# Optimization experiments

Hardware: AMD Instinct MI355X
Metric: run time of the kernel (lower is better)

## Reference

```python
import jax, jax.numpy as jnp
import numpy as np

DIM = 2048
KV_DIM = 1024
NUM_HEADS = 16
HEAD_DIM = DIM // NUM_HEADS  # 128
EPS = 1e-6
B, LQ, LKV = 2, 4096, 1024


def _rope_cos_sin(L, d, base=10000.0):
    inv_freq = 1.0 / (base ** (np.arange(0, d, 2, dtype=np.float32) / d))  # [d/2]
    freqs = np.arange(L, dtype=np.float32)[:, None] * inv_freq[None, :]   # [L, d/2]
    emb = np.concatenate([freqs, freqs], axis=-1)                          # [L, d]
    return jnp.asarray(np.cos(emb)), jnp.asarray(np.sin(emb))


def setup_inputs() -> dict:
    key = jax.random.key(0)
    ks = jax.random.split(key, 10)
    x = jax.random.normal(ks[0], (B, LQ, DIM), dtype=jnp.float32)
    y = jax.random.normal(ks[1], (B, LKV, KV_DIM), dtype=jnp.float32)
    xc, xs = _rope_cos_sin(LQ, HEAD_DIM)
    yc, ys = _rope_cos_sin(LKV, HEAD_DIM)
    x_cos = jnp.broadcast_to(xc[None], (B, LQ, HEAD_DIM))
    x_sin = jnp.broadcast_to(xs[None], (B, LQ, HEAD_DIM))
    y_cos = jnp.broadcast_to(yc[None], (B, LKV, HEAD_DIM))
    y_sin = jnp.broadcast_to(ys[None], (B, LKV, HEAD_DIM))
    s = 0.02
    Wq = jax.random.normal(ks[2], (DIM, DIM), dtype=jnp.float32) * s
    Wk = jax.random.normal(ks[3], (DIM, KV_DIM), dtype=jnp.float32) * s
    Wv = jax.random.normal(ks[4], (DIM, KV_DIM), dtype=jnp.float32) * s
    Wo = jax.random.normal(ks[5], (DIM, DIM), dtype=jnp.float32) * s
    bq = jnp.zeros((DIM,), jnp.float32)
    bk = jnp.zeros((DIM,), jnp.float32)
    bv = jnp.zeros((DIM,), jnp.float32)
    bo = jnp.zeros((DIM,), jnp.float32)
    rmsq_w = jnp.ones((DIM,), jnp.float32)
    rmsk_w = jnp.ones((DIM,), jnp.float32)
    ln_w = jnp.ones((KV_DIM,), jnp.float32)
    ln_b = jnp.zeros((KV_DIM,), jnp.float32)
    return dict(x=x, y=y, x_cos=x_cos, x_sin=x_sin, y_cos=y_cos, y_sin=y_sin,
                Wq=Wq, bq=bq, Wk=Wk, bk=bk, Wv=Wv, bv=bv, Wo=Wo, bo=bo,
                rmsq_w=rmsq_w, rmsk_w=rmsk_w, ln_w=ln_w, ln_b=ln_b)


def _rms_norm(t, w, eps=EPS):
    return t * jax.lax.rsqrt(jnp.mean(t * t, axis=-1, keepdims=True) + eps) * w


def _layer_norm(t, w, b, eps=EPS):
    mu = jnp.mean(t, axis=-1, keepdims=True)
    var = jnp.mean(jnp.square(t - mu), axis=-1, keepdims=True)
    return (t - mu) * jax.lax.rsqrt(var + eps) * w + b


def _rotate_half(t):
    d2 = t.shape[-1] // 2
    return jnp.concatenate([-t[..., d2:], t[..., :d2]], axis=-1)


def _apply_rope(t, cos, sin):
    # t: [B, L, H, D]; cos/sin: [B, L, D] -> unsqueeze head dim (unsqueeze_dim=2)
    cos = cos[:, :, None, :]
    sin = sin[:, :, None, :]
    return t * cos + _rotate_half(t) * sin


def _block_forward(x, y, x_cos, x_sin, y_cos, y_sin,
                   Wq, bq, Wk, bk, Wv, bv, Wo, bo,
                   rmsq_w, rmsk_w, ln_w, ln_b):
    Bb, Lq, D = x.shape
    Lk = y.shape[1]
    H, Dh = NUM_HEADS, HEAD_DIM
    # y pre-norm (block-level LayerNorm)
    yn = _layer_norm(y, ln_w, ln_b)
    # projections + RMSNorm on q/k
    q = _rms_norm(x @ Wq.T + bq, rmsq_w)   # [B, Lq, D]
    k = _rms_norm(yn @ Wk.T + bk, rmsk_w)  # [B, Lk, D]
    v = yn @ Wv.T + bv                     # [B, Lk, D]
    # split heads and apply RoPE
    q = _apply_rope(q.reshape(Bb, Lq, H, Dh), x_cos, x_sin)
    k = _apply_rope(k.reshape(Bb, Lk, H, Dh), y_cos, y_sin)
    v = v.reshape(Bb, Lk, H, Dh)
    # non-causal cross attention, scale = 1/sqrt(head_dim)
    scale = 1.0 / jnp.sqrt(jnp.asarray(Dh, q.dtype))
    scores = jnp.einsum('blhd,bmhd->bhlm', q, k) * scale
    probs = jax.nn.softmax(scores, axis=-1)
    out = jnp.einsum('bhlm,bmhd->blhd', probs, v).reshape(Bb, Lq, D)
    return out @ Wo.T + bo


def reference(x, y, x_cos, x_sin, y_cos, y_sin,
              Wq, bq, Wk, bk, Wv, bv, Wo, bo,
              rmsq_w, rmsk_w, ln_w, ln_b):
    return _block_forward(x, y, x_cos, x_sin, y_cos, y_sin,
                          Wq, bq, Wk, bk, Wv, bv, Wo, bo,
                          rmsq_w, rmsk_w, ln_w, ln_b)
```

## Files before the change

### kernel.cpp

```cpp
#include <hip/hip_runtime.h>


typedef __attribute__((ext_vector_type(8))) short    short8;
typedef __attribute__((ext_vector_type(8))) unsigned short ushort8;
typedef __attribute__((ext_vector_type(4))) unsigned short ushort4v;
typedef __attribute__((ext_vector_type(4))) float    f32x4;
typedef __attribute__((ext_vector_type(16))) float   f32x16;
typedef __attribute__((ext_vector_type(4))) unsigned int uint4v;

#define DEV __device__ __forceinline__

DEV unsigned short f2bf(float f) {
  unsigned int u = __builtin_bit_cast(unsigned int, f);
  u += 0x7FFFu + ((u >> 16) & 1u);
  return (unsigned short)(u >> 16);
}
DEV float bf2f(unsigned short h) {
  return __builtin_bit_cast(float, ((unsigned int)h) << 16);
}
DEV unsigned int cvtpk_bf16(float lo, float hi) {
  unsigned int r;
  asm("v_cvt_pk_bf16_f32 %0, %1, %2" : "=v"(r) : "v"(lo), "v"(hi));
  return r;
}
DEV short8 mk8(unsigned a, unsigned b, unsigned c, unsigned d) {
  uint4v t; t.x = a; t.y = b; t.z = c; t.w = d;
  return __builtin_bit_cast(short8, t);
}

DEV void gload_lds16(const void* g, void* l) {
  __builtin_amdgcn_global_load_lds(
      (const __attribute__((address_space(1))) void*)g,
      (__attribute__((address_space(3))) void*)l, 16, 0, 0);
}

__global__ __launch_bounds__(256) void prep_kernel(const float* __restrict__ y,
                                                   const float* __restrict__ lnw,
                                                   const float* __restrict__ lnb,
                                                   unsigned short* __restrict__ yn,
                                                   const float* __restrict__ x,
                                                   const float* __restrict__ Wq,
                                                   const float* __restrict__ Wk,
                                                   const float* __restrict__ Wv,
                                                   const float* __restrict__ Wo,
                                                   unsigned short* __restrict__ xb,
                                                   unsigned short* __restrict__ Wqb,
                                                   unsigned short* __restrict__ Wkb,
                                                   unsigned short* __restrict__ Wvb,
                                                   unsigned short* __restrict__ Wob) {
  const int t = threadIdx.x;
  if (blockIdx.x < 2048) {
    const int row = blockIdx.x;
    const float* yr = y + (size_t)row * 1024;
    float4 v = *(const float4*)(yr + t * 4);
    float s1 = v.x + v.y + v.z + v.w;
    float s2 = v.x * v.x + v.y * v.y + v.z * v.z + v.w * v.w;
#pragma unroll
    for (int m = 1; m < 64; m <<= 1) {
      s1 += __shfl_xor(s1, m);
      s2 += __shfl_xor(s2, m);
    }
    __shared__ float red[8];
    const int wave = t >> 6, lane = t & 63;
    if (lane == 0) { red[wave] = s1; red[4 + wave] = s2; }
    __syncthreads();
    s1 = red[0] + red[1] + red[2] + red[3];
    s2 = red[4] + red[5] + red[6] + red[7];
    const float mu = s1 * (1.0f / 1024.0f);
    const float var = s2 * (1.0f / 1024.0f) - mu * mu;
    const float rs = rsqrtf(var + 1e-6f);
    ushort4v o;
    o.x = f2bf((v.x - mu) * rs * lnw[t * 4 + 0] + lnb[t * 4 + 0]);
    o.y = f2bf((v.y - mu) * rs * lnw[t * 4 + 1] + lnb[t * 4 + 1]);
    o.z = f2bf((v.z - mu) * rs * lnw[t * 4 + 2] + lnb[t * 4 + 2]);
    o.w = f2bf((v.w - mu) * rs * lnw[t * 4 + 3] + lnb[t * 4 + 3]);
    *(ushort4v*)(yn + (size_t)row * 1024 + t * 4) = o;
    return;
  }
  const int nx = 4194304, nwq = 1048576, nwk = 524288, nwv = 524288;
  const int total = 7340032;
  int i = (blockIdx.x - 2048) * 256 + t;
  const int stride = 1536 * 256;
  for (; i < total; i += stride) {
    int j = i;
    const float* s; unsigned short* d;
    if (j < nx) { s = x; d = xb; }
    else if ((j -= nx) < nwq) { s = Wq; d = Wqb; }
    else if ((j -= nwq) < nwk) { s = Wk; d = Wkb; }
    else if ((j -= nwk) < nwv) { s = Wv; d = Wvb; }
    else { j -= nwv; s = Wo; d = Wob; }
    float4 v = *(const float4*)(s + (size_t)j * 4);
    ushort4v o;
    o.x = f2bf(v.x); o.y = f2bf(v.y); o.z = f2bf(v.z); o.w = f2bf(v.w);
    *(ushort4v*)(d + (size_t)j * 4) = o;
  }
}

template <int EPI>
DEV void gemm256_body(const unsigned short* __restrict__ A,
                      const unsigned short* __restrict__ W,
                      const float* __restrict__ bias0,
                      const float* __restrict__ bias1,
                      int nsplit, void* __restrict__ Cout,
                      int M, int N, int K, int ldRow,
                      int bidLocal, int nwg, char* ldsb, int tid) {
  const int wave = tid >> 6, lane = tid & 63;
  const int l31 = lane & 31, hi = lane >> 5;
  const int wm = wave >> 2, wn = wave & 3;

  const int wgid = (bidLocal & 7) * (nwg >> 3) + (bidLocal >> 3);
  const int nbn = N >> 8;
  const int m0 = (wgid / nbn) * 256;
  const int n0 = (wgid % nbn) * 256;

  const char* Ab = (const char*)A;
  const char* Wb = (const char*)W;
  const size_t ld = (size_t)ldRow * 2;
  const int NT = K >> 6;
  const int NI = NT >> 1;

  const int prow2 = tid >> 4;
  const int psw   = ((tid * 16) & 255) ^ ((prow2 & 15) << 4);
  const int pdst  = tid * 16;
  const char* pAg = Ab + (size_t)(m0 + 2 * prow2 + (psw >> 7)) * ld + (psw & 127);
  const char* pBg = Wb + (size_t)(n0 + 2 * prow2 + (psw >> 7)) * ld + (psw & 127);

  f32x16 acc[4][2] = {};
  short8 af[2][4];
  short8 bf[2][4];

#define LDSB(BUF, SEG) (ldsb + ((BUF) * 4 + (SEG)) * 16384)

#define STG(BUF, HALF, ISB, TAU) do {                                         \
    const char* _g = ((ISB) ? pBg : pAg) + (size_t)(HALF) * 128 * ld +        \
                     (size_t)(TAU) * 128;                                     \
    char* _l = LDSB(BUF, (ISB) * 2 + (HALF));                                 \
    gload_lds16(_g, _l + pdst);                                               \
    gload_lds16(_g + 64 * ld, _l + pdst + 8192);                              \
  } while (0)

#define LDA(BUF, H) do {                                                      \
    const char* _b = LDSB(BUF, wm);                                           \
    _Pragma("unroll") for (int mf = 0; mf < 2; ++mf) {                        \
      const int ar = (H) * 64 + mf * 32 + l31;                                \
      const int _r = ar >> 1;                                                 \
      const int swz = (_r & 15) << 4;                                         \
      _Pragma("unroll") for (int ks = 0; ks < 4; ++ks)                        \
        af[mf][ks] = *(const short8*)(_b + _r * 256 +                         \
                       (((ar & 1) * 128 + ks * 32 + hi * 16) ^ swz));         \
    }                                                                         \
  } while (0)

#define LDB(BUF, G) do {                                                      \
    const char* _b = LDSB(BUF, 2 + (wn >> 1));                                \
    const int br = (wn & 1) * 64 + (G) * 32 + l31;                            \
    const int _r = br >> 1;                                                   \
    const int swz = (_r & 15) << 4;                                           \
    _Pragma("unroll") for (int ks = 0; ks < 4; ++ks)                          \
      bf[G][ks] = *(const short8*)(_b + _r * 256 +                            \
                     (((br & 1) * 128 + ks * 32 + hi * 16) ^ swz));           \
  } while (0)

#define MFMA_Q(H, G) do {                                                     \
    __builtin_amdgcn_s_setprio(1);                                            \
    _Pragma("unroll") for (int ks = 0; ks < 4; ++ks)                          \
    _Pragma("unroll") for (int mf = 0; mf < 2; ++mf)                          \
      acc[(H) * 2 + mf][G] =                                                  \
        __builtin_amdgcn_mfma_f32_32x32x16_bf16(af[mf][ks], bf[G][ks],        \
                                                acc[(H) * 2 + mf][G], 0,0,0); \
    __builtin_amdgcn_s_setprio(0);                                            \
  } while (0)

#define BAR() __builtin_amdgcn_s_barrier()
#define VM4() asm volatile("s_waitcnt vmcnt(4)" ::: "memory")
#define VM0() asm volatile("s_waitcnt vmcnt(0)" ::: "memory")

  STG(0, 0, 0, 0); STG(0, 1, 0, 0); STG(0, 0, 1, 0); STG(0, 1, 1, 0);
  STG(1, 0, 1, 1); STG(1, 1, 1, 1);
  VM4(); BAR();

  for (int t = 0; t < NI - 1; ++t) {
    const int t2 = 2 * t;
    LDA(0, 0); LDB(0, 0); STG(1, 0, 0, t2 + 1);
    BAR(); MFMA_Q(0, 0); BAR();
    LDB(0, 1); STG(1, 1, 0, t2 + 1);
    BAR(); MFMA_Q(0, 1); BAR();
    LDA(0, 1); STG(0, 0, 1, t2 + 2);
    BAR(); MFMA_Q(1, 1); BAR();
    STG(0, 1, 1, t2 + 2);
    BAR(); MFMA_Q(1, 0); VM4(); BAR();
    LDA(1, 0); LDB(1, 0); STG(0, 0, 0, t2 + 2);
    BAR(); MFMA_Q(0, 0); BAR();
    LDB(1, 1); STG(0, 1, 0, t2 + 2);
    BAR(); MFMA_Q(0, 1); BAR();
    LDA(1, 1); STG(1, 0, 1, t2 + 3);
    BAR(); MFMA_Q(1, 1); BAR();
    STG(1, 1, 1, t2 + 3);
    BAR(); MFMA_Q(1, 0); VM4(); BAR();
  }

  LDA(0, 0); LDB(0, 0); STG(1, 0, 0, NT - 1);
  BAR(); MFMA_Q(0, 0); BAR();
  LDB(0, 1); STG(1, 1, 0, NT - 1);
  BAR(); MFMA_Q(0, 1); BAR();
  LDA(0, 1);
  BAR(); MFMA_Q(1, 1); BAR();
  BAR(); MFMA_Q(1, 0); VM0(); BAR();
  LDA(1, 0); LDB(1, 0); MFMA_Q(0, 0);
  LDB(1, 1); MFMA_Q(0, 1);
  LDA(1, 1); MFMA_Q(1, 1);
  MFMA_Q(1, 0);

#undef STG
#undef LDA
#undef LDB
#undef MFMA_Q
#undef BAR
#undef VM4
#undef VM0
#undef LDSB

#pragma unroll
  for (int nf = 0; nf < 2; ++nf) {
    const int n = n0 + wn * 64 + nf * 32 + l31;
    float bv = 0.f;
    if constexpr (EPI != 2) bv = (n < nsplit) ? bias0[n] : bias1[n - nsplit];
#pragma unroll
    for (int mfr = 0; mfr < 4; ++mfr) {
      const int mB = m0 + wm * 128 + mfr * 32 + 4 * hi;
#pragma unroll
      for (int r = 0; r < 16; ++r) {
        const int row = mB + (r & 3) + 8 * (r >> 2);
        const float v = acc[mfr][nf][r] + bv;
        if constexpr (EPI == 1)
          ((float*)Cout)[(size_t)row * N + n] = v;
        else
          ((unsigned short*)Cout)[(size_t)row * N + n] = f2bf(v);
      }
    }
  }
}

__global__ __launch_bounds__(512, 2) void gemm_dual(const unsigned short* __restrict__ xb,
                                                    const unsigned short* __restrict__ Wqb,
                                                    const float* __restrict__ bq,
                                                    unsigned short* __restrict__ qpre,
                                                    const unsigned short* __restrict__ ynb,
                                                    const unsigned short* __restrict__ Wkb,
                                                    unsigned short* __restrict__ kvpA,
                                                    unsigned short* __restrict__ kvpB) {
  __shared__ __align__(16) char lds[2][4][16384];
  gemm256_body<0>(xb, Wqb, bq, bq, 2048, qpre, 8192, 2048, 2048, 2048,
                  blockIdx.x, 256, &lds[0][0][0], threadIdx.x);
  __syncthreads();
  const int kvt = blockIdx.x & 127, khalf = blockIdx.x >> 7;
  gemm256_body<2>(ynb + khalf * 512, Wkb + khalf * 512, nullptr, nullptr, 0,
                  khalf ? kvpB : kvpA, 2048, 4096, 512, 1024,
                  kvt, 128, &lds[0][0][0], threadIdx.x);
}

__global__ __launch_bounds__(512, 2) void gemm_f32(const unsigned short* __restrict__ A,
                                                   const unsigned short* __restrict__ W,
                                                   const float* __restrict__ bias,
                                                   float* __restrict__ C,
                                                   int M, int N, int K) {
  __shared__ __align__(16) char lds[2][4][16384];
  gemm256_body<1>(A, W, bias, bias, N, C, M, N, K, K,
                  blockIdx.x, 256, &lds[0][0][0], threadIdx.x);
}

DEV void rmsrope2_body(const unsigned short* __restrict__ in,
                       const unsigned short* __restrict__ in2,
                       const float* __restrict__ bias,
                       const float* __restrict__ w,
                       const float* __restrict__ cs,
                       const float* __restrict__ sn,
                       unsigned short* __restrict__ out,
                       int L, int ldin, float scale, int row,
                       float* srow, float* red) {
  const int t = threadIdx.x;
  ushort8 v = *(const ushort8*)(in + (size_t)row * ldin + t * 8);
  float vals[8];
  if (in2) {
    ushort8 v2 = *(const ushort8*)(in2 + (size_t)row * ldin + t * 8);
#pragma unroll
    for (int j = 0; j < 8; ++j) vals[j] = bf2f(v[j]) + bf2f(v2[j]) + bias[t * 8 + j];
  } else {
#pragma unroll
    for (int j = 0; j < 8; ++j) vals[j] = bf2f(v[j]);
  }
  float ss = 0.f;
#pragma unroll
  for (int j = 0; j < 8; ++j) { ss += vals[j] * vals[j]; srow[t * 8 + j] = vals[j]; }
#pragma unroll
  for (int m = 1; m < 64; m <<= 1) ss += __shfl_xor(ss, m);
  const int wave = t >> 6, lane = t & 63;
  if (lane == 0) red[wave] = ss;
  __syncthreads();
  const float tot = red[0] + red[1] + red[2] + red[3];
  const float rms = rsqrtf(tot * (1.0f / 2048.0f) + 1e-6f);

  const int n0 = t * 8;
  const int d0 = n0 & 127;
  const int hh = n0 >> 7;
  const float sign = (d0 < 64) ? -1.0f : 1.0f;
  const float* cb = cs + (size_t)row * 128 + d0;
  const float* sb = sn + (size_t)row * 128 + d0;
  ushort8 ou;
#pragma unroll
  for (int j = 0; j < 8; ++j) {
    const float self = vals[j] * rms * w[n0 + j];
    const float part = srow[(n0 ^ 64) + j] * rms * w[(n0 ^ 64) + j];
    ou[j] = f2bf((self * cb[j] + sign * part * sb[j]) * scale);
  }
  const int b = row / L, l = row - (row / L) * L;
  *(ushort8*)(out + (((size_t)(b * 16 + hh)) * L + l) * 128 + d0) = ou;
}

DEV void vtrans2_body(const unsigned short* __restrict__ va,
                      const unsigned short* __restrict__ vb,
                      const float* __restrict__ bv,
                      unsigned short* __restrict__ vt, int ldv, int bid,
                      unsigned short (*lt)[130]) {
  const int kt = bid & 15, bh = bid >> 4;
  const int h = bh & 15, b = bh >> 4;
  const int t = threadIdx.x;
  const int i0 = t >> 4, c0 = (t & 15) * 8;
  const size_t sbase = ((size_t)(b * 1024 + kt * 64)) * ldv + h * 128;
#pragma unroll
  for (int ii = 0; ii < 4; ++ii) {
    const int i = i0 + ii * 16;
    ushort8 a = *(const ushort8*)(va + sbase + (size_t)i * ldv + c0);
    ushort8 bb = *(const ushort8*)(vb + sbase + (size_t)i * ldv + c0);
#pragma unroll
    for (int j = 0; j < 8; ++j)
      lt[i][c0 + j] = f2bf(bf2f(a[j]) + bf2f(bb[j]) + bv[h * 128 + c0 + j]);
  }
  __syncthreads();
  const int d0 = t >> 3, j0 = (t & 7) * 8;
  unsigned short* dst = vt + (size_t)bh * 128 * 1024 + kt * 64;
#pragma unroll
  for (int dd = 0; dd < 4; ++dd) {
    const int d = d0 + dd * 32;
    ushort8 o;
#pragma unroll
    for (int jj = 0; jj < 8; ++jj) o[jj] = lt[j0 + jj][d];
    *(ushort8*)(dst + (size_t)d * 1024 + j0) = o;
  }
}

__global__ __launch_bounds__(256) void post_kernel(const unsigned short* __restrict__ qpre,
                                                   const float* __restrict__ rmsq_w,
                                                   const float* __restrict__ x_cos,
                                                   const float* __restrict__ x_sin,
                                                   unsigned short* __restrict__ qr,
                                                   const unsigned short* __restrict__ kvpA,
                                                   const unsigned short* __restrict__ kvpB,
                                                   const float* __restrict__ bk,
                                                   const float* __restrict__ bv,
                                                   const float* __restrict__ rmsk_w,
                                                   const float* __restrict__ y_cos,
                                                   const float* __restrict__ y_sin,
                                                   unsigned short* __restrict__ kr,
                                                   unsigned short* __restrict__ vt,
                                                   float qscale) {
  __shared__ __align__(16) float srow[2048];
  __shared__ float red[4];
  __shared__ unsigned short lt[64][130];
  const int b = blockIdx.x;
  if (b < 8192) {
    rmsrope2_body(qpre, nullptr, nullptr, rmsq_w, x_cos, x_sin, qr,
                  4096, 2048, qscale, b, srow, red);
  } else if (b < 10240) {
    rmsrope2_body(kvpA, kvpB, bk, rmsk_w, y_cos, y_sin, kr,
                  1024, 4096, 1.0f, b - 8192, srow, red);
  } else {
    vtrans2_body(kvpA + 2048, kvpB + 2048, bv, vt, 4096, b - 10240, lt);
  }
}

__global__ __launch_bounds__(256, 2) void attn_kernel(const unsigned short* __restrict__ q,
                                                      const unsigned short* __restrict__ k,
                                                      const unsigned short* __restrict__ vt,
                                                      unsigned short* __restrict__ ao) {
  __shared__ __align__(16) char sK[2][64 * 256];
  __shared__ __align__(16) char sV[2][64 * 256];

  const int bid0 = blockIdx.x;
  const int bid = (bid0 & 7) * 128 + (bid0 >> 3);
  const int qt = bid & 31, bh = bid >> 5;
  const int tid = threadIdx.x;
  const int wave = tid >> 6, lane = tid & 63;
  const int l31 = lane & 31, hi = lane >> 5;

  const unsigned short* qbase = q + (((size_t)bh * 4096) + qt * 128 + wave * 32) * 128;
  const char* kbase = (const char*)(k + (size_t)bh * 1024 * 128);
  const char* vbase = (const char*)(vt + (size_t)bh * 128 * 1024);

  short8 qb[8];
#pragma unroll
  for (int step = 0; step < 8; ++step)
    qb[step] = *(const short8*)(qbase + (size_t)l31 * 128 + step * 16 + hi * 8);

  f32x16 o[4] = {};
  float lsum = 0.f;

#define STAGE_KV(BUF, KV0) do {                                              \
    _Pragma("unroll")                                                        \
    for (int i = 0; i < 4; ++i) {                                            \
      const int p = (i * 256 + tid) * 16;                                    \
      const int row = p >> 8;                                                \
      const int si = (p & 255) ^ ((row & 15) << 4);                          \
      gload_lds16(kbase + (size_t)((KV0) + row) * 256 + si, sK[BUF] + p);    \
    }                                                                        \
    _Pragma("unroll")                                                        \
    for (int i = 0; i < 4; ++i) {                                            \
      const int p = (i * 256 + tid) * 16;                                    \
      const int row = p >> 8;                                                \
      const int si = (p & 255) ^ ((row & 15) << 4);                          \
      const int d = 2 * row + (si >> 7);                                     \
      gload_lds16(vbase + (size_t)d * 2048 + (KV0) * 2 + (si & 127),         \
                  sV[BUF] + p);                                              \
    }                                                                        \
  } while (0)

#define QK(K, S0, S1) do {                                                   \
    const int ksw = (l31 & 15) << 4;                                         \
    _Pragma("unroll") for (int step = 0; step < 8; ++step) {                 \
      const int cb2 = step * 32 + hi * 16;                                   \
      short8 kf0 = *(const short8*)((K) + l31 * 256 + (cb2 ^ ksw));          \
      short8 kf1 = *(const short8*)((K) + (32 + l31) * 256 + (cb2 ^ ksw));   \
      S0 = __builtin_amdgcn_mfma_f32_32x32x16_bf16(kf0, qb[step], S0, 0,0,0);\
      S1 = __builtin_amdgcn_mfma_f32_32x32x16_bf16(kf1, qb[step], S1, 0,0,0);\
    }                                                                        \
  } while (0)

#define SOFTMAX_PV(V, SS, F) do {                                            \
    float p_[16];                                                            \
    _Pragma("unroll") for (int r = 0; r < 16; ++r) p_[r] = exp2f((SS)[r]);   \
    lsum += (((p_[0]+p_[1])+(p_[2]+p_[3])) + ((p_[4]+p_[5])+(p_[6]+p_[7])))  \
          + (((p_[8]+p_[9])+(p_[10]+p_[11])) + ((p_[12]+p_[13])+(p_[14]+p_[15])));\
    unsigned w0 = cvtpk_bf16(p_[0], p_[1]),  w1 = cvtpk_bf16(p_[2], p_[3]),  \
             w2 = cvtpk_bf16(p_[4], p_[5]),  w3 = cvtpk_bf16(p_[6], p_[7]),  \
             w4 = cvtpk_bf16(p_[8], p_[9]),  w5 = cvtpk_bf16(p_[10], p_[11]),\
             w6 = cvtpk_bf16(p_[12], p_[13]),w7 = cvtpk_bf16(p_[14], p_[15]);\
    asm volatile("v_permlane32_swap_b32 %0, %1" : "+v"(w0), "+v"(w2));       \
    asm volatile("v_permlane32_swap_b32 %0, %1" : "+v"(w1), "+v"(w3));       \
    asm volatile("v_permlane32_swap_b32 %0, %1" : "+v"(w4), "+v"(w6));       \
    asm volatile("v_permlane32_swap_b32 %0, %1" : "+v"(w5), "+v"(w7));       \
    const short8 fr0 = mk8(w0, w1, w2, w3);                                  \
    const short8 fr1 = mk8(w4, w5, w6, w7);                                  \
    _Pragma("unroll") for (int kstep = 0; kstep < 2; ++kstep) {              \
      const short8 pa = kstep ? fr1 : fr0;                                   \
      const int colb = (F) * 64 + kstep * 32 + hi * 16;                      \
      _Pragma("unroll") for (int dt = 0; dt < 4; ++dt) {                     \
        const int vrow = dt * 16 + (l31 >> 1);                               \
        const int inner = (l31 & 1) * 128 + colb;                            \
        short8 vf = *(const short8*)((V) + vrow * 256 +                      \
                                     (inner ^ ((vrow & 15) << 4)));          \
        o[dt] = __builtin_amdgcn_mfma_f32_32x32x16_bf16(pa, vf, o[dt], 0,0,0);\
      }                                                                      \
    }                                                                        \
  } while (0)

#define TILE(BUF) do {                                                       \
    f32x16 s0 = {}, s1 = {};                                                 \
    QK(sK[BUF], s0, s1);                                                     \
    SOFTMAX_PV(sV[BUF], s0, 0);                                              \
    SOFTMAX_PV(sV[BUF], s1, 1);                                              \
  } while (0)

  STAGE_KV(0, 0);
  __syncthreads();

#pragma unroll 1
  for (int kt2 = 0; kt2 < 8; ++kt2) {
    STAGE_KV(1, (2 * kt2 + 1) * 64);
    TILE(0);
    __syncthreads();
    if (kt2 < 7) STAGE_KV(0, (2 * kt2 + 2) * 64);
    TILE(1);
    __syncthreads();
  }
#undef STAGE_KV
#undef QK
#undef SOFTMAX_PV
#undef TILE

  lsum += __shfl_xor(lsum, 32);
  const float linv = 1.0f / lsum;
  const int b = bh >> 4, h = bh & 15;
#pragma unroll
  for (int r = 0; r < 16; ++r) {
    const int crow = (r & 3) + 8 * (r >> 2) + 4 * hi;
    const float inv = __shfl(linv, crow);
    const int qg = qt * 128 + wave * 32 + crow;
    const size_t orow = ((size_t)b * 4096 + qg) * 2048 + h * 128;
#pragma unroll
    for (int dt = 0; dt < 4; ++dt)
      ao[orow + dt * 32 + l31] = f2bf(o[dt][r] * inv);
  }
}

extern "C" void kernel_launch(void* const* d_in, const int* in_sizes, int n_in,
                              void* d_out, int out_size, void* d_ws, size_t ws_size,
                              hipStream_t stream) {
  (void)in_sizes; (void)n_in; (void)out_size; (void)ws_size;
  const float* x      = (const float*)d_in[0];
  const float* y      = (const float*)d_in[1];
  const float* x_cos  = (const float*)d_in[2];
  const float* x_sin  = (const float*)d_in[3];
  const float* y_cos  = (const float*)d_in[4];
  const float* y_sin  = (const float*)d_in[5];
  const float* Wq     = (const float*)d_in[6];
  const float* bq     = (const float*)d_in[7];
  const float* Wk     = (const float*)d_in[8];
  const float* bk     = (const float*)d_in[9];
  const float* Wv     = (const float*)d_in[10];
  const float* bv     = (const float*)d_in[11];
  const float* Wo     = (const float*)d_in[12];
  const float* bo     = (const float*)d_in[13];
  const float* rmsq_w = (const float*)d_in[14];
  const float* rmsk_w = (const float*)d_in[15];
  const float* ln_w   = (const float*)d_in[16];
  const float* ln_b   = (const float*)d_in[17];

  char* ws = (char*)d_ws;
  unsigned short* xb    = (unsigned short*)(ws + 0);
  unsigned short* Wqb   = (unsigned short*)(ws + 33554432);
  unsigned short* Wkb   = (unsigned short*)(ws + 41943040);
  unsigned short* Wvb   = (unsigned short*)(ws + 46137344);
  unsigned short* Wob   = (unsigned short*)(ws + 50331648);
  unsigned short* ynb   = (unsigned short*)(ws + 58720256);
  unsigned short* qpre  = (unsigned short*)(ws + 62914560);
  unsigned short* kvpA  = (unsigned short*)(ws + 96468992);
  unsigned short* kvpB  = (unsigned short*)(ws + 113246208);
  unsigned short* qr    = xb;
  unsigned short* kr    = Wqb;
  unsigned short* vt    = Wkb;
  unsigned short* ao    = qpre;
  (void)Wvb;

  const float qscale = 1.4426950408889634f * 0.08838834764831843f;

  prep_kernel<<<3584, 256, 0, stream>>>(y, ln_w, ln_b, ynb, x, Wq, Wk, Wv, Wo,
                                        xb, Wqb, Wkb, Wvb, Wob);
  gemm_dual<<<256, 512, 0, stream>>>(xb, Wqb, bq, qpre, ynb, Wkb, kvpA, kvpB);
  post_kernel<<<10752, 256, 0, stream>>>(qpre, rmsq_w, x_cos, x_sin, qr,
                                         kvpA, kvpB, bk, bv, rmsk_w,
                                         y_cos, y_sin, kr, vt, qscale);
  attn_kernel<<<1024, 256, 0, stream>>>(qr, kr, vt, ao);
  gemm_f32<<<256, 512, 0, stream>>>(ao, Wob, bo, (float*)d_out, 8192, 2048, 2048);
}
```

Measured before the change: 306.2 us.

## Double per-wave query rows in attention to reuse K/V LDS fragments

Each attention wave now handles 64 query rows (two 32-row groups) instead of 32, so every K and V fragment read from LDS feeds two MFMAs. The grid is halved to 512 blocks and launch bounds drop to one block per CU occupancy target. This cuts LDS reads and K/V global staging per query row. In exchange it roughly doubles accumulator and Q register use, lowers occupancy, and leaves fewer blocks to fill the device.

```diff
diff --git a/kernel.cpp b/kernel.cpp
--- a/kernel.cpp
+++ b/kernel.cpp
@@ -379,7 +379,7 @@
   }
 }
 
-__global__ __launch_bounds__(256, 2) void attn_kernel(const unsigned short* __restrict__ q,
+__global__ __launch_bounds__(256, 1) void attn_kernel(const unsigned short* __restrict__ q,
                                                       const unsigned short* __restrict__ k,
                                                       const unsigned short* __restrict__ vt,
                                                       unsigned short* __restrict__ ao) {
@@ -387,23 +387,25 @@
   __shared__ __align__(16) char sV[2][64 * 256];
 
   const int bid0 = blockIdx.x;
-  const int bid = (bid0 & 7) * 128 + (bid0 >> 3);
-  const int qt = bid & 31, bh = bid >> 5;
+  const int bid = (bid0 & 7) * 64 + (bid0 >> 3);
+  const int qt = bid & 15, bh = bid >> 4;
   const int tid = threadIdx.x;
   const int wave = tid >> 6, lane = tid & 63;
   const int l31 = lane & 31, hi = lane >> 5;
 
-  const unsigned short* qbase = q + (((size_t)bh * 4096) + qt * 128 + wave * 32) * 128;
+  const unsigned short* qbase = q + (((size_t)bh * 4096) + qt * 256 + wave * 64) * 128;
   const char* kbase = (const char*)(k + (size_t)bh * 1024 * 128);
   const char* vbase = (const char*)(vt + (size_t)bh * 128 * 1024);
 
-  short8 qb[8];
-#pragma unroll
-  for (int step = 0; step < 8; ++step)
-    qb[step] = *(const short8*)(qbase + (size_t)l31 * 128 + step * 16 + hi * 8);
-
-  f32x16 o[4] = {};
-  float lsum = 0.f;
+  short8 qb[2][8];
+#pragma unroll
+  for (int g = 0; g < 2; ++g)
+#pragma unroll
+    for (int step = 0; step < 8; ++step)
+      qb[g][step] = *(const short8*)(qbase + (size_t)(g * 32 + l31) * 128 + step * 16 + hi * 8);
+
+  f32x16 o[2][4] = {};
+  float lsum[2] = {0.f, 0.f};
 
 #define STAGE_KV(BUF, KV0) do {                                              \
     _Pragma("unroll")                                                        \
@@ -424,22 +426,11 @@
     }                                                                        \
   } while (0)
 
-#define QK(K, S0, S1) do {                                                   \
-    const int ksw = (l31 & 15) << 4;                                         \
-    _Pragma("unroll") for (int step = 0; step < 8; ++step) {                 \
-      const int cb2 = step * 32 + hi * 16;                                   \
-      short8 kf0 = *(const short8*)((K) + l31 * 256 + (cb2 ^ ksw));          \
-      short8 kf1 = *(const short8*)((K) + (32 + l31) * 256 + (cb2 ^ ksw));   \
-      S0 = __builtin_amdgcn_mfma_f32_32x32x16_bf16(kf0, qb[step], S0, 0,0,0);\
-      S1 = __builtin_amdgcn_mfma_f32_32x32x16_bf16(kf1, qb[step], S1, 0,0,0);\
-    }                                                                        \
-  } while (0)
-
-#define SOFTMAX_PV(V, SS, F) do {                                            \
+#define SM(SS, G) do {                                                       \
     float p_[16];                                                            \
     _Pragma("unroll") for (int r = 0; r < 16; ++r) p_[r] = exp2f((SS)[r]);   \
-    lsum += (((p_[0]+p_[1])+(p_[2]+p_[3])) + ((p_[4]+p_[5])+(p_[6]+p_[7])))  \
-          + (((p_[8]+p_[9])+(p_[10]+p_[11])) + ((p_[12]+p_[13])+(p_[14]+p_[15])));\
+    lsum[G] += (((p_[0]+p_[1])+(p_[2]+p_[3])) + ((p_[4]+p_[5])+(p_[6]+p_[7])))\
+             + (((p_[8]+p_[9])+(p_[10]+p_[11])) + ((p_[12]+p_[13])+(p_[14]+p_[15])));\
     unsigned w0 = cvtpk_bf16(p_[0], p_[1]),  w1 = cvtpk_bf16(p_[2], p_[3]),  \
              w2 = cvtpk_bf16(p_[4], p_[5]),  w3 = cvtpk_bf16(p_[6], p_[7]),  \
              w4 = cvtpk_bf16(p_[8], p_[9]),  w5 = cvtpk_bf16(p_[10], p_[11]),\
@@ -448,26 +439,40 @@
     asm volatile("v_permlane32_swap_b32 %0, %1" : "+v"(w1), "+v"(w3));       \
     asm volatile("v_permlane32_swap_b32 %0, %1" : "+v"(w4), "+v"(w6));       \
     asm volatile("v_permlane32_swap_b32 %0, %1" : "+v"(w5), "+v"(w7));       \
-    const short8 fr0 = mk8(w0, w1, w2, w3);                                  \
-    const short8 fr1 = mk8(w4, w5, w6, w7);                                  \
+    frA[G] = mk8(w0, w1, w2, w3);                                            \
+    frB[G] = mk8(w4, w5, w6, w7);                                            \
+  } while (0)
+
+#define HALF(K, V, H) do {                                                   \
+    f32x16 s0 = {}, s1 = {};                                                 \
+    const int ksw = (l31 & 15) << 4;                                         \
+    _Pragma("unroll") for (int step = 0; step < 8; ++step) {                 \
+      const int cb2 = step * 32 + hi * 16;                                   \
+      short8 kf = *(const short8*)((K) + ((H) * 32 + l31) * 256 + (cb2 ^ ksw));\
+      s0 = __builtin_amdgcn_mfma_f32_32x32x16_bf16(kf, qb[0][step], s0, 0,0,0);\
+      s1 = __builtin_amdgcn_mfma_f32_32x32x16_bf16(kf, qb[1][step], s1, 0,0,0);\
+    }                                                                        \
+    SM(s0, 0);                                                               \
+    SM(s1, 1);                                                               \
     _Pragma("unroll") for (int kstep = 0; kstep < 2; ++kstep) {              \
-      const short8 pa = kstep ? fr1 : fr0;                                   \
-      const int colb = (F) * 64 + kstep * 32 + hi * 16;                      \
+      const short8 pa0 = kstep ? frB[0] : frA[0];                            \
+      const short8 pa1 = kstep ? frB[1] : frA[1];                            \
+      const int colb = (H) * 64 + kstep * 32 + hi * 16;                      \
       _Pragma("unroll") for (int dt = 0; dt < 4; ++dt) {                     \
         const int vrow = dt * 16 + (l31 >> 1);                               \
         const int inner = (l31 & 1) * 128 + colb;                            \
         short8 vf = *(const short8*)((V) + vrow * 256 +                      \
                                      (inner ^ ((vrow & 15) << 4)));          \
-        o[dt] = __builtin_amdgcn_mfma_f32_32x32x16_bf16(pa, vf, o[dt], 0,0,0);\
+        o[0][dt] = __builtin_amdgcn_mfma_f32_32x32x16_bf16(pa0, vf, o[0][dt], 0,0,0);\
+        o[1][dt] = __builtin_amdgcn_mfma_f32_32x32x16_bf16(pa1, vf, o[1][dt], 0,0,0);\
       }                                                                      \
     }                                                                        \
   } while (0)
 
 #define TILE(BUF) do {                                                       \
-    f32x16 s0 = {}, s1 = {};                                                 \
-    QK(sK[BUF], s0, s1);                                                     \
-    SOFTMAX_PV(sV[BUF], s0, 0);                                              \
-    SOFTMAX_PV(sV[BUF], s1, 1);                                              \
+    short8 frA[2], frB[2];                                                   \
+    HALF(sK[BUF], sV[BUF], 0);                                               \
+    HALF(sK[BUF], sV[BUF], 1);                                               \
   } while (0)
 
   STAGE_KV(0, 0);
@@ -483,22 +488,25 @@
     __syncthreads();
   }
 #undef STAGE_KV
-#undef QK
-#undef SOFTMAX_PV
+#undef SM
+#undef HALF
 #undef TILE
 
-  lsum += __shfl_xor(lsum, 32);
-  const float linv = 1.0f / lsum;
   const int b = bh >> 4, h = bh & 15;
 #pragma unroll
-  for (int r = 0; r < 16; ++r) {
-    const int crow = (r & 3) + 8 * (r >> 2) + 4 * hi;
-    const float inv = __shfl(linv, crow);
-    const int qg = qt * 128 + wave * 32 + crow;
-    const size_t orow = ((size_t)b * 4096 + qg) * 2048 + h * 128;
-#pragma unroll
-    for (int dt = 0; dt < 4; ++dt)
-      ao[orow + dt * 32 + l31] = f2bf(o[dt][r] * inv);
+  for (int g = 0; g < 2; ++g) {
+    const float tot = lsum[g] + __shfl_xor(lsum[g], 32);
+    const float linv = 1.0f / tot;
+#pragma unroll
+    for (int r = 0; r < 16; ++r) {
+      const int crow = (r & 3) + 8 * (r >> 2) + 4 * hi;
+      const float inv = __shfl(linv, crow);
+      const int qg = qt * 256 + wave * 64 + g * 32 + crow;
+      const size_t orow = ((size_t)b * 4096 + qg) * 2048 + h * 128;
+#pragma unroll
+      for (int dt = 0; dt < 4; ++dt)
+        ao[orow + dt * 32 + l31] = f2bf(o[g][dt][r] * inv);
+    }
   }
 }
 
@@ -549,6 +557,6 @@
   post_kernel<<<10752, 256, 0, stream>>>(qpre, rmsq_w, x_cos, x_sin, qr,
                                          kvpA, kvpB, bk, bv, rmsk_w,
                                          y_cos, y_sin, kr, vt, qscale);
-  attn_kernel<<<1024, 256, 0, stream>>>(qr, kr, vt, ao);
+  attn_kernel<<<512, 256, 0, stream>>>(qr, kr, vt, ao);
   gemm_f32<<<256, 512, 0, stream>>>(ao, Wob, bo, (float*)d_out, 8192, 2048, 2048);
 }
```

Measured after the change: 326.3 us. +6.6%, slower.
